# Kernel tuning notes

Measured on AMD Instinct MI355X. Metric: run time of the kernel, lower is better.

Reference implementation:

```python
import jax, jax.numpy as jnp
import numpy as np

B, C, H, W = 4, 512, 64, 64
D = C // 8  # query/key channels

def setup_inputs() -> dict:
    key = jax.random.key(0)
    ks = jax.random.split(key, 8)
    s = 0.05
    return {
        "x": jax.random.normal(ks[0], (B, C, H, W, 1), dtype=jnp.float32),
        "Wq": jax.random.normal(ks[1], (D, C), dtype=jnp.float32) * s,
        "bq": jax.random.normal(ks[2], (D,), dtype=jnp.float32) * s,
        "Wk": jax.random.normal(ks[3], (D, C), dtype=jnp.float32) * s,
        "bk": jax.random.normal(ks[4], (D,), dtype=jnp.float32) * s,
        "Wv": jax.random.normal(ks[5], (C, C), dtype=jnp.float32) * s,
        "bv": jax.random.normal(ks[6], (C,), dtype=jnp.float32) * s,
        "gamma": jax.random.normal(ks[7], (1,), dtype=jnp.float32),
    }

def reference(x, Wq, bq, Wk, bk, Wv, bv, gamma):
    b, c, h, w, _ = x.shape
    xs = x.reshape(b, c, h, w)
    flat = xs.reshape(b, c, h * w)                       # b c n
    # 1x1 convs are channel matmuls
    q = jnp.einsum('dc,bcn->bnd', Wq, flat) + bq         # b n d
    k = jnp.einsum('dc,bcn->bdn', Wk, flat) + bk[None, :, None]  # b d n
    energy = jnp.einsum('bnd,bdm->bnm', q, k)            # b n n (no 1/sqrt(d) scaling)
    attn = jax.nn.softmax(energy, axis=-1)
    v = jnp.einsum('ec,bcn->ben', Wv, flat) + bv[None, :, None]   # b c n
    out = jnp.einsum('ben,bmn->bem', v, attn)            # value @ attn^T
    out = gamma[0] * out.reshape(b, c, h, w) + xs
    return out.reshape(b, c, h, w, 1)
```

## Files before the change

### kernel.cpp

```cpp
#include <hip/hip_runtime.h>
#include <math.h>

using bf16x8 = __attribute__((ext_vector_type(8))) short;
using f32x4  = __attribute__((ext_vector_type(4))) float;

#define MFMA(a,b,c) __builtin_amdgcn_mfma_f32_16x16x32_bf16((a),(b),(c),0,0,0)

static constexpr int NB = 4, NC = 512, NN = 4096, ND = 64;
static constexpr float LOG2E = 1.4426950408889634f;

__device__ __forceinline__ short f2bf(float f) {
  union { float f; unsigned u; } v; v.f = f;
  unsigned r = v.u + 0x7FFFu + ((v.u >> 16) & 1u);
  return (short)(r >> 16);
}

__device__ __forceinline__ unsigned cvt_pk_bf16(float a, float b) {
  unsigned r;
  asm("v_cvt_pk_bf16_f32 %0, %1, %2" : "=v"(r) : "v"(a), "v"(b));
  return r;
}

__device__ __forceinline__ void gld16(void* lds, const void* g) {
  __builtin_amdgcn_global_load_lds(
      (const __attribute__((address_space(1))) unsigned*)g,
      (__attribute__((address_space(3))) unsigned*)lds, 16, 0, 0);
}

__global__ void cast_w(const float* Wq, const float* Wk, const float* Wv,
                       short* Wqb, short* Wkb, short* Wvb) {
  int i = blockIdx.x * 256 + threadIdx.x;
  if (i < ND * NC) { Wqb[i] = f2bf(Wq[i]); Wkb[i] = f2bf(Wk[i]); }
  if (i < NC * NC) { Wvb[i] = f2bf(Wv[i]); }
}

__global__ __launch_bounds__(256) void transpose_x(const float* x, short* xT) {
  int b = blockIdx.z, c0 = blockIdx.y * 32, n0 = blockIdx.x * 64;
  int tid = threadIdx.x;
  int n = n0 + (tid >> 2);
  int c = c0 + (tid & 3) * 8;
  const float* xb = x + (size_t)b * NC * NN;
  bf16x8 v;
  #pragma unroll
  for (int i = 0; i < 8; i++) v[i] = f2bf(xb[(size_t)(c + i) * NN + n]);
  *(bf16x8*)(xT + ((size_t)b * NN + n) * NC + c) = v;
}

__global__ __launch_bounds__(256) void proj_qk(const short* xT, const short* Wqb, const short* Wkb,
                        const float* bq, const float* bk, short* Q, short* K) {
  int b = blockIdx.y;
  int wave = threadIdx.x >> 6, lane = threadIdx.x & 63;
  int lc = lane & 15, grp = lane >> 4;
  int n0 = blockIdx.x * 64 + wave * 16;
  const short* xTb = xT + ((size_t)b * NN + n0) * NC;
  f32x4 accq[4] = {}, acck[4] = {};
  for (int c0 = 0; c0 < NC; c0 += 32) {
    bf16x8 a = *(const bf16x8*)(xTb + (size_t)lc * NC + c0 + grp * 8);
    #pragma unroll
    for (int di = 0; di < 4; di++) {
      bf16x8 wq = *(const bf16x8*)(Wqb + (size_t)(di * 16 + lc) * NC + c0 + grp * 8);
      bf16x8 wk = *(const bf16x8*)(Wkb + (size_t)(di * 16 + lc) * NC + c0 + grp * 8);
      accq[di] = MFMA(a, wq, accq[di]);
      acck[di] = MFMA(a, wk, acck[di]);
    }
  }
  short* Qb = Q + (size_t)b * NN * ND;
  short* Kb = K + (size_t)b * NN * ND;
  #pragma unroll
  for (int di = 0; di < 4; di++)
    #pragma unroll
    for (int j = 0; j < 4; j++) {
      int n = n0 + grp * 4 + j;
      int d = di * 16 + lc;
      Qb[(size_t)n * ND + d] = f2bf((accq[di][j] + bq[d]) * LOG2E);
      Kb[(size_t)n * ND + d] = f2bf(acck[di][j] + bk[d]);
    }
}

__global__ __launch_bounds__(256, 2) void proj_v(const short* xT, const short* Wvb,
                                                 const float* bv, short* V) {
  __shared__ char lds[65536];
  int b = blockIdx.z;
  int tid = threadIdx.x, wv = tid >> 6, lane = tid & 63;
  int lc = lane & 15, grp = lane >> 4;
  int e0 = blockIdx.y * 128;
  int n0 = blockIdx.x * 128;
  const char* Wg = (const char*)Wvb;
  const char* Xg = (const char*)(xT + (size_t)b * NN * NC);
  int eq = (wv >> 1) * 64, nq = (wv & 1) * 64;

  auto stage = [&](int t) {
    char* buf = lds + (t & 1) * 32768;
    int c0 = t * 64;
    #pragma unroll
    for (int i = 0; i < 4; i++) {
      int r = wv * 32 + i * 8 + (lane >> 3), g = lane & 7;
      gld16(buf + wv * 4096 + i * 1024 + lane * 16,
            Wg + (size_t)(e0 + r) * 1024 + (size_t)c0 * 2 + ((g ^ (r & 7)) * 16));
    }
    #pragma unroll
    for (int i = 0; i < 4; i++) {
      int r = wv * 32 + i * 8 + (lane >> 3), g = lane & 7;
      gld16(buf + 16384 + wv * 4096 + i * 1024 + lane * 16,
            Xg + (size_t)(n0 + r) * 1024 + (size_t)c0 * 2 + ((g ^ (r & 7)) * 16));
    }
  };

  f32x4 acc[4][4] = {};
  stage(0);
  for (int t = 0; t < 8; t++) {
    asm volatile("s_waitcnt vmcnt(0)" ::: "memory");
    __builtin_amdgcn_sched_barrier(0);
    __builtin_amdgcn_s_barrier();
    if (t < 7) stage(t + 1);
    const char* buf = lds + (t & 1) * 32768;
    bf16x8 wf[4][2], xf[4][2];
    #pragma unroll
    for (int mi = 0; mi < 4; mi++)
      #pragma unroll
      for (int ks = 0; ks < 2; ks++) {
        int r = eq + mi * 16 + lc;
        wf[mi][ks] = *(const bf16x8*)(buf + r * 128 + (((ks * 4 + grp) ^ (r & 7)) * 16));
      }
    #pragma unroll
    for (int ni = 0; ni < 4; ni++)
      #pragma unroll
      for (int ks = 0; ks < 2; ks++) {
        int r = nq + ni * 16 + lc;
        xf[ni][ks] = *(const bf16x8*)(buf + 16384 + r * 128 + (((ks * 4 + grp) ^ (r & 7)) * 16));
      }
    #pragma unroll
    for (int mi = 0; mi < 4; mi++)
      #pragma unroll
      for (int ni = 0; ni < 4; ni++) {
        acc[mi][ni] = MFMA(wf[mi][0], xf[ni][0], acc[mi][ni]);
        acc[mi][ni] = MFMA(wf[mi][1], xf[ni][1], acc[mi][ni]);
      }
  }
  short* Vbp = V + (size_t)b * NC * NN;
  #pragma unroll
  for (int mi = 0; mi < 4; mi++)
    #pragma unroll
    for (int j = 0; j < 4; j++) {
      int e = e0 + eq + mi * 16 + grp * 4 + j;
      float bb = bv[e];
      #pragma unroll
      for (int ni = 0; ni < 4; ni++) {
        int n = n0 + nq + ni * 16 + lc;
        Vbp[(size_t)e * NN + n] = f2bf(acc[mi][ni][j] + bb);
      }
    }
}

__global__ __launch_bounds__(256, 2) void attn_stats(const short* Q, const short* K,
                                                     float* Mp, float* Lp) {
  __shared__ char lds[16384];
  int b = blockIdx.y, nh = blockIdx.z;
  int tid = threadIdx.x, wave = tid >> 6, lane = tid & 63;
  int lc = lane & 15, grp = lane >> 4;
  int m0 = blockIdx.x * 128 + wave * 32;
  const short* Qb = Q + (size_t)b * NN * ND;
  const char* Kg = (const char*)(K + (size_t)b * NN * ND);

  int kR[2], kC[2];
  #pragma unroll
  for (int i = 0; i < 2; i++) {
    int A = (wave * 2 + i) * 1024 + lane * 16;
    kR[i] = A >> 7;
    kC[i] = ((A >> 4) & 7) ^ (kR[i] & 7);
  }
  auto stageK = [&](char* base0, int n0) {
    #pragma unroll
    for (int i = 0; i < 2; i++)
      gld16(base0 + (wave * 2 + i) * 1024,
            Kg + (size_t)(n0 + kR[i]) * 128 + kC[i] * 16);
  };

  bf16x8 qf[2][2];
  #pragma unroll
  for (int mi = 0; mi < 2; mi++)
    #pragma unroll
    for (int kk = 0; kk < 2; kk++)
      qf[mi][kk] = *(const bf16x8*)(Qb + (size_t)(m0 + mi * 16 + lc) * ND + kk * 32 + grp * 8);

  float rmax[2][4], rsum[2][4];
  #pragma unroll
  for (int mi = 0; mi < 2; mi++)
    #pragma unroll
    for (int j = 0; j < 4; j++) { rmax[mi][j] = -1e30f; rsum[mi][j] = 0.f; }

  stageK(lds, nh * 1024);
  __syncthreads();
  int cur = 0;
  for (int tt = 0; tt < 16; tt++) {
    int t = nh * 16 + tt;
    if (tt + 1 < 16) stageK(lds + (cur ^ 1) * 8192, (t + 1) * 64);
    const char* Kb_l = lds + cur * 8192;
    f32x4 s[2][4] = {};
    #pragma unroll
    for (int ni = 0; ni < 4; ni++) {
      int row = ni * 16 + lc;
      bf16x8 kf0 = *(const bf16x8*)(Kb_l + row * 128 + ((grp ^ (row & 7)) * 16));
      bf16x8 kf1 = *(const bf16x8*)(Kb_l + row * 128 + (((grp + 4) ^ (row & 7)) * 16));
      #pragma unroll
      for (int mi = 0; mi < 2; mi++) {
        s[mi][ni] = MFMA(qf[mi][0], kf0, s[mi][ni]);
        s[mi][ni] = MFMA(qf[mi][1], kf1, s[mi][ni]);
      }
    }
    #pragma unroll
    for (int mi = 0; mi < 2; mi++)
      #pragma unroll
      for (int j = 0; j < 4; j++) {
        float a0 = s[mi][0][j], a1 = s[mi][1][j], a2 = s[mi][2][j], a3 = s[mi][3][j];
        float m4 = fmaxf(fmaxf(a0, a1), fmaxf(a2, a3));
        float nm = fmaxf(rmax[mi][j], m4);
        rsum[mi][j] = rsum[mi][j] * exp2f(rmax[mi][j] - nm)
                    + exp2f(a0 - nm) + exp2f(a1 - nm) + exp2f(a2 - nm) + exp2f(a3 - nm);
        rmax[mi][j] = nm;
      }
    __syncthreads();
    cur ^= 1;
  }
  #pragma unroll
  for (int mi = 0; mi < 2; mi++)
    #pragma unroll
    for (int j = 0; j < 4; j++) {
      float gm = rmax[mi][j];
      for (int o = 1; o < 16; o <<= 1) gm = fmaxf(gm, __shfl_xor(gm, o));
      float ps = rsum[mi][j] * exp2f(rmax[mi][j] - gm);
      for (int o = 1; o < 16; o <<= 1) ps += __shfl_xor(ps, o);
      if (lc == 0) {
        int m = m0 + mi * 16 + grp * 4 + j;
        Mp[((size_t)nh * NB + b) * NN + m] = gm;
        Lp[((size_t)nh * NB + b) * NN + m] = ps;
      }
    }
}

__global__ void stats_combine(const float* Mp, const float* Lp, float* Mrow, float* Lrow) {
  int i = blockIdx.x * 256 + threadIdx.x;
  if (i >= NB * NN) return;
  float M = Mp[i];
  #pragma unroll
  for (int s = 1; s < 4; s++) M = fmaxf(M, Mp[(size_t)s * NB * NN + i]);
  float L = 0.f;
  #pragma unroll
  for (int s = 0; s < 4; s++)
    L += Lp[(size_t)s * NB * NN + i] * exp2f(Mp[(size_t)s * NB * NN + i] - M);
  Mrow[i] = M; Lrow[i] = L;
}

__global__ __launch_bounds__(256, 2) void attn_out_kernel(
    const short* Q, const short* K, const short* V,
    const float* Mrow, const float* Lrow, const float* x,
    const float* gamma, float* out) {
  __shared__ char lds[81920];
  int bid = blockIdx.x;
  int combo = bid & 7;
  int b = combo >> 1;
  int e0 = (combo & 1) * 256;
  int m0 = (bid >> 3) * 64;
  int tid = threadIdx.x, we = tid >> 6, lane = tid & 63;
  int lc = lane & 15, grp = lane >> 4;

  char* Kl = lds;
  char* Pl = lds + 8192;
  char* Vb0 = lds + 16384;

  const short* Qb = Q + (size_t)b * NN * ND;
  const char* Kg = (const char*)(K + (size_t)b * NN * ND);
  const char* Vg = (const char*)(V + (size_t)b * NC * NN);

  int kR[2], kC[2], vR[8], vC[8];
  #pragma unroll
  for (int i = 0; i < 2; i++) {
    int ch = i * 256 + tid;
    kR[i] = ch >> 3; kC[i] = (ch & 7) ^ (kR[i] & 7);
  }
  #pragma unroll
  for (int i = 0; i < 8; i++) {
    int ch = i * 256 + tid;
    vR[i] = ch >> 3; vC[i] = (ch & 7) ^ (vR[i] & 7);
  }
  auto stageK = [&](int n0) {
    #pragma unroll
    for (int i = 0; i < 2; i++)
      gld16(Kl + (i * 256 + tid) * 16, Kg + (size_t)(n0 + kR[i]) * 128 + kC[i] * 16);
  };
  auto stageV = [&](char* dst, int n0) {
    #pragma unroll
    for (int i = 0; i < 8; i++)
      gld16(dst + (i * 256 + tid) * 16,
            Vg + (size_t)(e0 + vR[i]) * 8192 + (size_t)n0 * 2 + vC[i] * 16);
  };

  bf16x8 qf[4][2];
  #pragma unroll
  for (int mi = 0; mi < 4; mi++)
    #pragma unroll
    for (int dk = 0; dk < 2; dk++)
      qf[mi][dk] = *(const bf16x8*)(Qb + (size_t)(m0 + mi * 16 + lc) * ND + dk * 32 + grp * 8);
  float Mr[4];
  #pragma unroll
  for (int mi = 0; mi < 4; mi++)
    Mr[mi] = Mrow[(size_t)b * NN + m0 + mi * 16 + lc];

  f32x4 acc[4][4] = {};

  stageK(0);
  stageV(Vb0, 0);
  __syncthreads();
  for (int t = 0; t < 64; t++) {
    const char* Vl = Vb0 + (t & 1) * 32768;
    int krow = we * 16 + lc;
    bf16x8 kf0 = *(const bf16x8*)(Kl + krow * 128 + ((grp ^ (krow & 7)) * 16));
    bf16x8 kf1 = *(const bf16x8*)(Kl + krow * 128 + (((4 + grp) ^ (krow & 7)) * 16));
    #pragma unroll
    for (int mi = 0; mi < 4; mi++) {
      f32x4 s = {-Mr[mi], -Mr[mi], -Mr[mi], -Mr[mi]};
      s = MFMA(kf0, qf[mi][0], s);
      s = MFMA(kf1, qf[mi][1], s);
      unsigned w0 = cvt_pk_bf16(exp2f(s[0]), exp2f(s[1]));
      unsigned w1 = cvt_pk_bf16(exp2f(s[2]), exp2f(s[3]));
      int prow = mi * 16 + lc;
      char* base = Pl + prow * 128 + (((2 * we + (grp >> 1)) ^ (prow & 7)) << 4) + (grp & 1) * 8;
      *(unsigned*)base = w0;
      *(unsigned*)(base + 4) = w1;
    }
    __syncthreads();
    if (t < 63) {
      stageK((t + 1) * 64);
      stageV(Vb0 + ((t + 1) & 1) * 32768, (t + 1) * 64);
    }
    bf16x8 pa[4][2];
    #pragma unroll
    for (int mi = 0; mi < 4; mi++)
      #pragma unroll
      for (int ks = 0; ks < 2; ks++) {
        int prow = mi * 16 + lc;
        pa[mi][ks] = *(const bf16x8*)(Pl + prow * 128 + (((ks * 4 + grp) ^ (prow & 7)) * 16));
      }
    #pragma unroll
    for (int ei = 0; ei < 4; ei++) {
      int vrow = we * 64 + ei * 16 + lc;
      bf16x8 v0 = *(const bf16x8*)(Vl + vrow * 128 + ((grp ^ (vrow & 7)) * 16));
      bf16x8 v1 = *(const bf16x8*)(Vl + vrow * 128 + (((4 + grp) ^ (vrow & 7)) * 16));
      #pragma unroll
      for (int mi = 0; mi < 4; mi++) {
        acc[mi][ei] = MFMA(pa[mi][0], v0, acc[mi][ei]);
        acc[mi][ei] = MFMA(pa[mi][1], v1, acc[mi][ei]);
      }
    }
    __syncthreads();
  }

  float Li[4][4];
  #pragma unroll
  for (int mi = 0; mi < 4; mi++)
    #pragma unroll
    for (int j = 0; j < 4; j++)
      Li[mi][j] = 1.0f / Lrow[(size_t)b * NN + m0 + mi * 16 + grp * 4 + j];
  const float* xb = x + (size_t)b * NC * NN;
  float* ob = out + (size_t)b * NC * NN;
  float g = gamma[0];
  #pragma unroll
  for (int mi = 0; mi < 4; mi++)
    #pragma unroll
    for (int ei = 0; ei < 4; ei++) {
      int e = e0 + we * 64 + ei * 16 + lc;
      int mbase = m0 + mi * 16 + grp * 4;
      f32x4 xv = *(const f32x4*)(xb + (size_t)e * NN + mbase);
      f32x4 r;
      #pragma unroll
      for (int j = 0; j < 4; j++)
        r[j] = g * (acc[mi][ei][j] * Li[mi][j]) + xv[j];
      *(f32x4*)(ob + (size_t)e * NN + mbase) = r;
    }
}

extern "C" void kernel_launch(void* const* d_in, const int* in_sizes, int n_in,
                              void* d_out, int out_size, void* d_ws, size_t ws_size,
                              hipStream_t stream) {
  const float* x     = (const float*)d_in[0];
  const float* Wq    = (const float*)d_in[1];
  const float* bq    = (const float*)d_in[2];
  const float* Wk    = (const float*)d_in[3];
  const float* bk    = (const float*)d_in[4];
  const float* Wv    = (const float*)d_in[5];
  const float* bv    = (const float*)d_in[6];
  const float* gamma = (const float*)d_in[7];
  float* out = (float*)d_out;

  char* ws = (char*)d_ws;
  size_t off = 0;
  auto alloc = [&](size_t bytes) {
    void* p = ws + off;
    off = (off + bytes + 255) & ~(size_t)255;
    return p;
  };
  short* xT   = (short*)alloc((size_t)NB * NN * NC * 2);
  short* Wqb  = (short*)alloc((size_t)ND * NC * 2);
  short* Wkb  = (short*)alloc((size_t)ND * NC * 2);
  short* Wvb  = (short*)alloc((size_t)NC * NC * 2);
  short* Qb   = (short*)alloc((size_t)NB * NN * ND * 2);
  short* Kb   = (short*)alloc((size_t)NB * NN * ND * 2);
  short* Vb   = (short*)alloc((size_t)NB * NC * NN * 2);
  float* Mrow = (float*)alloc((size_t)NB * NN * 4);
  float* Lrow = (float*)alloc((size_t)NB * NN * 4);
  float* Mp   = (float*)alloc((size_t)4 * NB * NN * 4);
  float* Lp   = (float*)alloc((size_t)4 * NB * NN * 4);

  cast_w<<<dim3(1024), dim3(256), 0, stream>>>(Wq, Wk, Wv, Wqb, Wkb, Wvb);
  transpose_x<<<dim3(NN / 64, NC / 32, NB), dim3(256), 0, stream>>>(x, xT);
  proj_qk<<<dim3(NN / 64, NB), dim3(256), 0, stream>>>(xT, Wqb, Wkb, bq, bk, Qb, Kb);
  proj_v<<<dim3(NN / 128, NC / 128, NB), dim3(256), 0, stream>>>(xT, Wvb, bv, Vb);
  attn_stats<<<dim3(NN / 128, NB, 4), dim3(256), 0, stream>>>(Qb, Kb, Mp, Lp);
  stats_combine<<<dim3(NB * NN / 256), dim3(256), 0, stream>>>(Mp, Lp, Mrow, Lrow);
  attn_out_kernel<<<dim3(512), dim3(256), 0, stream>>>(
      Qb, Kb, Vb, Mrow, Lrow, x, gamma, out);
}
```

Measured before the change: 183.2 us.

## Load K and V fragments directly from global, double-buffer P, drop second barrier

The attention output kernel no longer stages K and V tiles through LDS with async global-to-LDS copies. Each wave now reads its K and V MFMA fragments straight from global memory into registers, with K prefetched one iteration ahead. LDS shrinks to a double-buffered P tile, which removes the trailing barrier, and the PV MFMA block runs under raised wave priority. This cuts LDS footprint and synchronisation, which may allow more blocks per CU, but it adds register pressure and less-coalesced, latency-exposed global loads for V that are no longer shared across waves.

```diff
diff --git a/kernel.cpp b/kernel.cpp
--- a/kernel.cpp
+++ b/kernel.cpp
@@ -255,7 +255,7 @@
     const short* Q, const short* K, const short* V,
     const float* Mrow, const float* Lrow, const float* x,
     const float* gamma, float* out) {
-  __shared__ char lds[81920];
+  __shared__ char Pl[16384];
   int bid = blockIdx.x;
   int combo = bid & 7;
   int b = combo >> 1;
@@ -264,37 +264,10 @@
   int tid = threadIdx.x, we = tid >> 6, lane = tid & 63;
   int lc = lane & 15, grp = lane >> 4;
 
-  char* Kl = lds;
-  char* Pl = lds + 8192;
-  char* Vb0 = lds + 16384;
-
   const short* Qb = Q + (size_t)b * NN * ND;
   const char* Kg = (const char*)(K + (size_t)b * NN * ND);
   const char* Vg = (const char*)(V + (size_t)b * NC * NN);
 
-  int kR[2], kC[2], vR[8], vC[8];
-  #pragma unroll
-  for (int i = 0; i < 2; i++) {
-    int ch = i * 256 + tid;
-    kR[i] = ch >> 3; kC[i] = (ch & 7) ^ (kR[i] & 7);
-  }
-  #pragma unroll
-  for (int i = 0; i < 8; i++) {
-    int ch = i * 256 + tid;
-    vR[i] = ch >> 3; vC[i] = (ch & 7) ^ (vR[i] & 7);
-  }
-  auto stageK = [&](int n0) {
-    #pragma unroll
-    for (int i = 0; i < 2; i++)
-      gld16(Kl + (i * 256 + tid) * 16, Kg + (size_t)(n0 + kR[i]) * 128 + kC[i] * 16);
-  };
-  auto stageV = [&](char* dst, int n0) {
-    #pragma unroll
-    for (int i = 0; i < 8; i++)
-      gld16(dst + (i * 256 + tid) * 16,
-            Vg + (size_t)(e0 + vR[i]) * 8192 + (size_t)n0 * 2 + vC[i] * 16);
-  };
-
   bf16x8 qf[4][2];
   #pragma unroll
   for (int mi = 0; mi < 4; mi++)
@@ -308,14 +281,18 @@
 
   f32x4 acc[4][4] = {};
 
-  stageK(0);
-  stageV(Vb0, 0);
-  __syncthreads();
+  bf16x8 kf0 = *(const bf16x8*)(Kg + (size_t)(we * 16 + lc) * 128 + grp * 16);
+  bf16x8 kf1 = *(const bf16x8*)(Kg + (size_t)(we * 16 + lc) * 128 + 64 + grp * 16);
+
   for (int t = 0; t < 64; t++) {
-    const char* Vl = Vb0 + (t & 1) * 32768;
-    int krow = we * 16 + lc;
-    bf16x8 kf0 = *(const bf16x8*)(Kl + krow * 128 + ((grp ^ (krow & 7)) * 16));
-    bf16x8 kf1 = *(const bf16x8*)(Kl + krow * 128 + (((4 + grp) ^ (krow & 7)) * 16));
+    char* Pw = Pl + (t & 1) * 8192;
+    bf16x8 vf[4][2];
+    #pragma unroll
+    for (int ei = 0; ei < 4; ei++)
+      #pragma unroll
+      for (int ks = 0; ks < 2; ks++)
+        vf[ei][ks] = *(const bf16x8*)(
+            Vg + (size_t)(e0 + we * 64 + ei * 16 + lc) * 8192 + t * 128 + ks * 64 + grp * 16);
     #pragma unroll
     for (int mi = 0; mi < 4; mi++) {
       f32x4 s = {-Mr[mi], -Mr[mi], -Mr[mi], -Mr[mi]};
@@ -324,35 +301,34 @@
       unsigned w0 = cvt_pk_bf16(exp2f(s[0]), exp2f(s[1]));
       unsigned w1 = cvt_pk_bf16(exp2f(s[2]), exp2f(s[3]));
       int prow = mi * 16 + lc;
-      char* base = Pl + prow * 128 + (((2 * we + (grp >> 1)) ^ (prow & 7)) << 4) + (grp & 1) * 8;
-      *(unsigned*)base = w0;
-      *(unsigned*)(base + 4) = w1;
+      int g = (2 * we + (grp >> 1)) ^ (prow & 7);
+      uint2 wv; wv.x = w0; wv.y = w1;
+      *(uint2*)(Pw + prow * 128 + g * 16 + (grp & 1) * 8) = wv;
+    }
+    {
+      int tn = (t + 1) & 63;
+      const char* kp = Kg + (size_t)(tn * 64 + we * 16 + lc) * 128;
+      kf0 = *(const bf16x8*)(kp + grp * 16);
+      kf1 = *(const bf16x8*)(kp + 64 + grp * 16);
     }
     __syncthreads();
-    if (t < 63) {
-      stageK((t + 1) * 64);
-      stageV(Vb0 + ((t + 1) & 1) * 32768, (t + 1) * 64);
-    }
     bf16x8 pa[4][2];
     #pragma unroll
     for (int mi = 0; mi < 4; mi++)
       #pragma unroll
       for (int ks = 0; ks < 2; ks++) {
-        int prow = mi * 16 + lc;
-        pa[mi][ks] = *(const bf16x8*)(Pl + prow * 128 + (((ks * 4 + grp) ^ (prow & 7)) * 16));
-      }
-    #pragma unroll
-    for (int ei = 0; ei < 4; ei++) {
-      int vrow = we * 64 + ei * 16 + lc;
-      bf16x8 v0 = *(const bf16x8*)(Vl + vrow * 128 + ((grp ^ (vrow & 7)) * 16));
-      bf16x8 v1 = *(const bf16x8*)(Vl + vrow * 128 + (((4 + grp) ^ (vrow & 7)) * 16));
+        int row = mi * 16 + lc;
+        pa[mi][ks] = *(const bf16x8*)(Pw + row * 128 + (((ks * 4 + grp) ^ (row & 7)) * 16));
+      }
+    __builtin_amdgcn_s_setprio(1);
+    #pragma unroll
+    for (int ei = 0; ei < 4; ei++)
       #pragma unroll
       for (int mi = 0; mi < 4; mi++) {
-        acc[mi][ei] = MFMA(pa[mi][0], v0, acc[mi][ei]);
-        acc[mi][ei] = MFMA(pa[mi][1], v1, acc[mi][ei]);
-      }
-    }
-    __syncthreads();
+        acc[mi][ei] = MFMA(pa[mi][0], vf[ei][0], acc[mi][ei]);
+        acc[mi][ei] = MFMA(pa[mi][1], vf[ei][1], acc[mi][ei]);
+      }
+    __builtin_amdgcn_s_setprio(0);
   }
 
   float Li[4][4];
```

Measured after the change: 233.8 us. 1.28x slower.

## Software-pipeline QK/exp with PV via double-buffered P and register K loads

Applied to the files above, without the earlier changes.

Drops the K staging through LDS and loads each wave's K fragment directly from global into registers one tile ahead. P is now double-buffered, so the QK^T MFMAs and exp for tile t+1 run after the PV MFMAs of tile t, leaving one barrier per iteration instead of two. The PV MFMA block is wrapped in s_setprio to favour matrix work across waves. It adds register pressure from prefetched K, and the global K loads are unswizzled and uncoalesced compared with the old LDS path.

```diff
diff --git a/kernel.cpp b/kernel.cpp
--- a/kernel.cpp
+++ b/kernel.cpp
@@ -264,30 +264,19 @@
   int tid = threadIdx.x, we = tid >> 6, lane = tid & 63;
   int lc = lane & 15, grp = lane >> 4;
 
-  char* Kl = lds;
-  char* Pl = lds + 8192;
+  char* Pl  = lds;
   char* Vb0 = lds + 16384;
 
   const short* Qb = Q + (size_t)b * NN * ND;
   const char* Kg = (const char*)(K + (size_t)b * NN * ND);
   const char* Vg = (const char*)(V + (size_t)b * NC * NN);
 
-  int kR[2], kC[2], vR[8], vC[8];
-  #pragma unroll
-  for (int i = 0; i < 2; i++) {
-    int ch = i * 256 + tid;
-    kR[i] = ch >> 3; kC[i] = (ch & 7) ^ (kR[i] & 7);
-  }
+  int vR[8], vC[8];
   #pragma unroll
   for (int i = 0; i < 8; i++) {
     int ch = i * 256 + tid;
     vR[i] = ch >> 3; vC[i] = (ch & 7) ^ (vR[i] & 7);
   }
-  auto stageK = [&](int n0) {
-    #pragma unroll
-    for (int i = 0; i < 2; i++)
-      gld16(Kl + (i * 256 + tid) * 16, Kg + (size_t)(n0 + kR[i]) * 128 + kC[i] * 16);
-  };
   auto stageV = [&](char* dst, int n0) {
     #pragma unroll
     for (int i = 0; i < 8; i++)
@@ -308,39 +297,53 @@
 
   f32x4 acc[4][4] = {};
 
-  stageK(0);
-  stageV(Vb0, 0);
-  __syncthreads();
-  for (int t = 0; t < 64; t++) {
-    const char* Vl = Vb0 + (t & 1) * 32768;
-    int krow = we * 16 + lc;
-    bf16x8 kf0 = *(const bf16x8*)(Kl + krow * 128 + ((grp ^ (krow & 7)) * 16));
-    bf16x8 kf1 = *(const bf16x8*)(Kl + krow * 128 + (((4 + grp) ^ (krow & 7)) * 16));
+  auto qk_to_P = [&](int t, bf16x8 k0, bf16x8 k1) {
+    char* Pw = Pl + (t & 1) * 8192;
     #pragma unroll
     for (int mi = 0; mi < 4; mi++) {
       f32x4 s = {-Mr[mi], -Mr[mi], -Mr[mi], -Mr[mi]};
-      s = MFMA(kf0, qf[mi][0], s);
-      s = MFMA(kf1, qf[mi][1], s);
+      s = MFMA(k0, qf[mi][0], s);
+      s = MFMA(k1, qf[mi][1], s);
       unsigned w0 = cvt_pk_bf16(exp2f(s[0]), exp2f(s[1]));
       unsigned w1 = cvt_pk_bf16(exp2f(s[2]), exp2f(s[3]));
       int prow = mi * 16 + lc;
-      char* base = Pl + prow * 128 + (((2 * we + (grp >> 1)) ^ (prow & 7)) << 4) + (grp & 1) * 8;
-      *(unsigned*)base = w0;
-      *(unsigned*)(base + 4) = w1;
-    }
+      int g = (2 * we + (grp >> 1)) ^ (prow & 7);
+      uint2 wv; wv.x = w0; wv.y = w1;
+      *(uint2*)(Pw + prow * 128 + g * 16 + (grp & 1) * 8) = wv;
+    }
+  };
+
+  stageV(Vb0, 0);
+  {
+    const char* kp = Kg + (size_t)(we * 16 + lc) * 128;
+    bf16x8 k0 = *(const bf16x8*)(kp + grp * 16);
+    bf16x8 k1 = *(const bf16x8*)(kp + 64 + grp * 16);
     __syncthreads();
+    qk_to_P(0, k0, k1);
+  }
+  __syncthreads();
+
+  for (int t = 0; t < 64; t++) {
+    const char* Vl = Vb0 + (t & 1) * 32768;
+    char* Pw = Pl + (t & 1) * 8192;
+
+    bf16x8 kn0 = {}, kn1 = {};
     if (t < 63) {
-      stageK((t + 1) * 64);
       stageV(Vb0 + ((t + 1) & 1) * 32768, (t + 1) * 64);
-    }
+      const char* kp = Kg + (size_t)((t + 1) * 64 + we * 16 + lc) * 128;
+      kn0 = *(const bf16x8*)(kp + grp * 16);
+      kn1 = *(const bf16x8*)(kp + 64 + grp * 16);
+    }
+
     bf16x8 pa[4][2];
     #pragma unroll
     for (int mi = 0; mi < 4; mi++)
       #pragma unroll
       for (int ks = 0; ks < 2; ks++) {
-        int prow = mi * 16 + lc;
-        pa[mi][ks] = *(const bf16x8*)(Pl + prow * 128 + (((ks * 4 + grp) ^ (prow & 7)) * 16));
-      }
+        int row = mi * 16 + lc;
+        pa[mi][ks] = *(const bf16x8*)(Pw + row * 128 + (((ks * 4 + grp) ^ (row & 7)) * 16));
+      }
+    __builtin_amdgcn_s_setprio(1);
     #pragma unroll
     for (int ei = 0; ei < 4; ei++) {
       int vrow = we * 64 + ei * 16 + lc;
@@ -352,6 +355,10 @@
         acc[mi][ei] = MFMA(pa[mi][1], v1, acc[mi][ei]);
       }
     }
+    __builtin_amdgcn_s_setprio(0);
+
+    if (t < 63) qk_to_P(t + 1, kn0, kn1);
+
     __syncthreads();
   }
 
```

Measured after the change: 184.8 us. Within noise of the previous version (+0.8%).
